# Kernel tuning notes

Measured on AMD Instinct MI355X. Metric: run time of the kernel, lower is better.

The kernel has to match this reference:

```python
import jax, jax.numpy as jnp
import numpy as np

D_MODEL = 256
N_HEADS = 8
N_LEVELS = 4
N_POINTS = 4
SHAPES = np.array([[64, 64], [32, 32], [16, 16], [8, 8]], dtype=np.int32)


def setup_inputs() -> dict:
    key = jax.random.key(0)
    ks = jax.random.split(key, 10)
    Lq = int((SHAPES[:, 0] * SHAPES[:, 1]).sum())  # 5440
    N, d = 8, D_MODEL
    noff = N_HEADS * N_LEVELS * N_POINTS * 2
    nw = N_HEADS * N_LEVELS * N_POINTS
    s = 1.0 / np.sqrt(d).astype(np.float32)
    inp = {
        'query': jax.random.normal(ks[0], (N, Lq, d), jnp.float32),
        'reference_points': jax.random.uniform(ks[1], (N, Lq, N_LEVELS, 2), jnp.float32),
        'spatial_shapes': jnp.asarray(SHAPES),
        'level_start_index': jnp.asarray(np.concatenate([[0], np.cumsum(SHAPES[:, 0] * SHAPES[:, 1])[:-1]]).astype(np.int32)),
        'W_value': jax.random.normal(ks[2], (d, d), jnp.float32) * s,
        'b_value': jnp.zeros((d,), jnp.float32),
        'W_off': jax.random.normal(ks[3], (d, noff), jnp.float32) * 0.01,
        'b_off': jax.random.uniform(ks[4], (noff,), jnp.float32, minval=-0.5, maxval=0.5),
        'W_attn': jax.random.normal(ks[5], (d, nw), jnp.float32) * s,
        'b_attn': jnp.zeros((nw,), jnp.float32),
        'W_out': jax.random.normal(ks[6], (d, d), jnp.float32) * s,
        'b_out': jnp.zeros((d,), jnp.float32),
    }
    return inp


def _bilinear_sample(val_l, loc_l, H, W):
    # val_l: [N, h, H*W, dh] flattened level feature map
    # loc_l: [N, Lq, h, P, 2] normalized (x, y) in [0, 1]
    # grid_sample semantics, align_corners=False, zero padding
    N, h, HW, dh = val_l.shape
    Lq, P = loc_l.shape[1], loc_l.shape[3]
    x = loc_l[..., 0] * W - 0.5
    y = loc_l[..., 1] * H - 0.5
    x0 = jnp.floor(x)
    y0 = jnp.floor(y)
    wx = (x - x0)[..., None]  # [N, Lq, h, P, 1]
    wy = (y - y0)[..., None]
    x0i = x0.astype(jnp.int32)
    y0i = y0.astype(jnp.int32)

    def gather(yi, xi):
        valid = (xi >= 0) & (xi < W) & (yi >= 0) & (yi < H)  # [N, Lq, h, P]
        idx = jnp.clip(yi, 0, H - 1) * W + jnp.clip(xi, 0, W - 1)
        idx = idx.transpose(0, 2, 1, 3).reshape(N, h, Lq * P)  # [N, h, Lq*P]
        g = jnp.take_along_axis(val_l, jnp.broadcast_to(idx[..., None], (N, h, Lq * P, dh)), axis=2)
        g = g.reshape(N, h, Lq, P, dh)
        mask = valid.transpose(0, 2, 1, 3)[..., None].astype(val_l.dtype)
        return g * mask

    v00 = gather(y0i, x0i)
    v01 = gather(y0i, x0i + 1)
    v10 = gather(y0i + 1, x0i)
    v11 = gather(y0i + 1, x0i + 1)
    wxt = wx.transpose(0, 2, 1, 3, 4)  # [N, h, Lq, P, 1]
    wyt = wy.transpose(0, 2, 1, 3, 4)
    return (v00 * (1 - wxt) * (1 - wyt) + v01 * wxt * (1 - wyt)
            + v10 * (1 - wxt) * wyt + v11 * wxt * wyt)  # [N, h, Lq, P, dh]


def reference(query, reference_points, spatial_shapes, level_start_index,
              W_value, b_value, W_off, b_off, W_attn, b_attn, W_out, b_out):
    shapes = np.asarray(spatial_shapes)  # static level shapes
    N, Lq, d = query.shape
    h, L, P = N_HEADS, N_LEVELS, N_POINTS
    dh = d // h

    v = query @ W_value + b_value  # value_proj (source reassigns query = value_proj(query))
    off = (v @ W_off + b_off).reshape(N, Lq, h, L, P, 2)
    aw = jax.nn.softmax((v @ W_attn + b_attn).reshape(N, Lq, h, L * P), axis=-1)
    aw = aw.reshape(N, Lq, h, L, P)

    # offset_normalizer = [W_l, H_l]
    norm = jnp.asarray(np.stack([shapes[:, 1], shapes[:, 0]], -1), dtype=v.dtype)  # [L, 2]
    loc = reference_points[:, :, None, :, None, :] + off / norm[None, None, None, :, None, :]

    val = v.reshape(N, Lq, h, dh).transpose(0, 2, 1, 3)  # [N, h, Lv, dh]
    out = jnp.zeros((N, h, Lq, dh), v.dtype)
    start = 0
    for l in range(L):
        H, W = int(shapes[l, 0]), int(shapes[l, 1])
        val_l = val[:, :, start:start + H * W]
        sampled = _bilinear_sample(val_l, loc[:, :, :, l], H, W)  # [N, h, Lq, P, dh]
        w_l = aw[:, :, :, l].transpose(0, 2, 1, 3)[..., None]  # [N, h, Lq, P, 1]
        out = out + (sampled * w_l).sum(axis=3)
        start += H * W

    out = out.transpose(0, 2, 1, 3).reshape(N, Lq, d)
    return out @ W_out + b_out
```

## Files before the change

### kernel.cpp

```cpp
#include <hip/hip_runtime.h>
#include <hip/hip_bf16.h>
#include <cstdint>
#include <cstddef>

#define NB 8
#define LQ 5440
#define MROWS (NB * LQ)

typedef __attribute__((ext_vector_type(8))) _Float16       f16x8;
typedef __attribute__((ext_vector_type(4))) float          f32x4;
typedef __attribute__((ext_vector_type(8))) unsigned short ushort8_t;

__device__ __forceinline__ unsigned short f2h(float f) {
    _Float16 h = (_Float16)f;
    unsigned short u;
    __builtin_memcpy(&u, &h, 2);
    return u;
}
__device__ __forceinline__ float h2f(unsigned short u) {
    _Float16 h;
    __builtin_memcpy(&h, &u, 2);
    return (float)h;
}

__global__ __launch_bounds__(256) void prep_weights(
    const float* __restrict__ Wv, const float* __restrict__ Woff,
    const float* __restrict__ Wat, const float* __restrict__ Wo,
    unsigned short* __restrict__ WvT, unsigned short* __restrict__ WoaT,
    unsigned short* __restrict__ WoT)
{
    const int id = blockIdx.x * 256 + threadIdx.x;
    if (id < 65536) {
        const int n = id >> 8, k = id & 255;
        WvT[id] = f2h(Wv[k * 256 + n]);
    } else if (id < 65536 + 98304) {
        const int p = id - 65536;
        const int n = p >> 8, k = p & 255;
        WoaT[p] = (n < 256) ? f2h(Woff[k * 256 + n])
                            : f2h(Wat[k * 128 + (n - 256)]);
    } else {
        const int p = id - (65536 + 98304);
        const int n = p >> 8, k = p & 255;
        WoT[p] = f2h(Wo[k * 256 + n]);
    }
}

#define LDT 40

template<bool A_FP32, bool F16_OUT>
__global__ __launch_bounds__(256) void gemm_mfma(
    const void* __restrict__ Ap, const unsigned short* __restrict__ Bt,
    const float* __restrict__ bias0, const float* __restrict__ bias1,
    void* __restrict__ C0, void* __restrict__ C1,
    int cs0, int cs1, int split)
{
    __shared__ unsigned short As[128 * LDT];
    __shared__ unsigned short Bs[128 * LDT];

    const int bm = blockIdx.y * 128;
    const int bn = blockIdx.x * 128;
    const int t    = threadIdx.x;
    const int lane = t & 63;
    const int wid  = t >> 6;
    const int wm   = (wid >> 1) * 64;
    const int wn   = (wid & 1) * 64;
    const int c    = lane & 15;
    const int qq   = lane >> 4;

    const int tr = t >> 1;
    const int kh = (t & 1) * 16;

    f32x4 acc[4][4];
#pragma unroll
    for (int i = 0; i < 4; ++i)
#pragma unroll
        for (int j = 0; j < 4; ++j)
            acc[i][j] = (f32x4){0.f, 0.f, 0.f, 0.f};

    for (int k0 = 0; k0 < 256; k0 += 32) {
        if (A_FP32) {
            const float4* Af = reinterpret_cast<const float4*>(
                (const float*)Ap + (size_t)(bm + tr) * 256 + k0 + kh);
            const float4 a0 = Af[0], a1 = Af[1], a2 = Af[2], a3 = Af[3];
            ushort8_t u0, u1;
            u0[0]=f2h(a0.x); u0[1]=f2h(a0.y); u0[2]=f2h(a0.z); u0[3]=f2h(a0.w);
            u0[4]=f2h(a1.x); u0[5]=f2h(a1.y); u0[6]=f2h(a1.z); u0[7]=f2h(a1.w);
            u1[0]=f2h(a2.x); u1[1]=f2h(a2.y); u1[2]=f2h(a2.z); u1[3]=f2h(a2.w);
            u1[4]=f2h(a3.x); u1[5]=f2h(a3.y); u1[6]=f2h(a3.z); u1[7]=f2h(a3.w);
            *reinterpret_cast<ushort8_t*>(&As[tr * LDT + kh])     = u0;
            *reinterpret_cast<ushort8_t*>(&As[tr * LDT + kh + 8]) = u1;
        } else {
            const ushort8_t* Ab = reinterpret_cast<const ushort8_t*>(
                (const unsigned short*)Ap + (size_t)(bm + tr) * 256 + k0 + kh);
            *reinterpret_cast<ushort8_t*>(&As[tr * LDT + kh])     = Ab[0];
            *reinterpret_cast<ushort8_t*>(&As[tr * LDT + kh + 8]) = Ab[1];
        }
        {
            const ushort8_t* Bb = reinterpret_cast<const ushort8_t*>(
                Bt + (size_t)(bn + tr) * 256 + k0 + kh);
            *reinterpret_cast<ushort8_t*>(&Bs[tr * LDT + kh])     = Bb[0];
            *reinterpret_cast<ushort8_t*>(&Bs[tr * LDT + kh + 8]) = Bb[1];
        }
        __syncthreads();

        f16x8 af[4], bfr[4];
#pragma unroll
        for (int i = 0; i < 4; ++i)
            af[i] = *reinterpret_cast<const f16x8*>(
                &As[(wm + i * 16 + c) * LDT + qq * 8]);
#pragma unroll
        for (int j = 0; j < 4; ++j)
            bfr[j] = *reinterpret_cast<const f16x8*>(
                &Bs[(wn + j * 16 + c) * LDT + qq * 8]);
#pragma unroll
        for (int i = 0; i < 4; ++i)
#pragma unroll
            for (int j = 0; j < 4; ++j)
                acc[i][j] = __builtin_amdgcn_mfma_f32_16x16x32_f16(
                    af[i], bfr[j], acc[i][j], 0, 0, 0);
        __syncthreads();
    }

#pragma unroll
    for (int j = 0; j < 4; ++j) {
        const int col    = bn + wn + j * 16 + c;
        const bool second = col >= split;
        const int ccol   = second ? col - split : col;
        const float bv   = second ? bias1[ccol] : bias0[ccol];
#pragma unroll
        for (int i = 0; i < 4; ++i) {
#pragma unroll
            for (int r = 0; r < 4; ++r) {
                const int row = bm + wm + i * 16 + qq * 4 + r;
                const float v0 = acc[i][j][r] + bv;
                if (F16_OUT) {
                    const float v1 = __shfl_xor(v0, 1);
                    if ((lane & 1) == 0) {
                        const unsigned int packed =
                            (unsigned int)f2h(v0) | ((unsigned int)f2h(v1) << 16);
                        unsigned short* Cb = (unsigned short*)(second ? C1 : C0);
                        const int cs = second ? cs1 : cs0;
                        *reinterpret_cast<unsigned int*>(
                            Cb + (size_t)row * cs + ccol) = packed;
                    }
                } else {
                    float* Cf = (float*)C0;
                    Cf[(size_t)row * cs0 + col] = v0;
                }
            }
        }
    }
}

__global__ __launch_bounds__(256) void sample_kernel(
    const unsigned short* __restrict__ v16,
    const unsigned short* __restrict__ off16,
    const unsigned short* __restrict__ attn16,
    const float* __restrict__ refpts,
    unsigned short* __restrict__ pre16)
{
    const int lane = threadIdx.x & 63;
    const int wv   = threadIdx.x >> 6;
    const int row  = blockIdx.x * 4 + wv;
    const int n    = row / LQ;

    __shared__ float4 sW[4][136];
    __shared__ int4   sI[4][136];

    const ushort4 o4 = reinterpret_cast<const ushort4*>(off16)[(size_t)row * 64 + lane];
    const unsigned int lg = reinterpret_cast<const unsigned int*>(attn16)[(size_t)row * 64 + lane];
    const float l0 = h2f((unsigned short)(lg & 0xffff));
    const float l1 = h2f((unsigned short)(lg >> 16));

    const int h   = lane >> 3;
    const int k   = lane & 7;
    const int j0  = 2 * k;
    const int lev = j0 >> 2;
    const float rx = refpts[(size_t)row * 8 + lev * 2 + 0];
    const float ry = refpts[(size_t)row * 8 + lev * 2 + 1];

    float m = fmaxf(l0, l1);
    m = fmaxf(m, __shfl_xor(m, 1));
    m = fmaxf(m, __shfl_xor(m, 2));
    m = fmaxf(m, __shfl_xor(m, 4));
    const float e0 = __expf(l0 - m);
    const float e1 = __expf(l1 - m);
    float s = e0 + e1;
    s += __shfl_xor(s, 1);
    s += __shfl_xor(s, 2);
    s += __shfl_xor(s, 4);
    const float inv = 1.f / s;

    const int  W     = 64 >> lev;
    const int  start = (lev == 0) ? 0 : (lev == 1) ? 4096 : (lev == 2) ? 5120 : 5376;
    const float rs   = 0.015625f * (float)(1 << lev);

#pragma unroll
    for (int pp = 0; pp < 2; ++pp) {
        const float lx = rx + h2f(pp ? o4.z : o4.x) * rs;
        const float ly = ry + h2f(pp ? o4.w : o4.y) * rs;
        const float wgt = (pp ? e1 : e0) * inv;

        const float x = lx * (float)W - 0.5f;
        const float y = ly * (float)W - 0.5f;
        const float fx = floorf(x), fy = floorf(y);
        const int xi = (int)fx, yi = (int)fy;
        const float wx = x - fx, wy = y - fy;

        const int x0 = min(max(xi, 0), W - 1);
        const int x1 = min(max(xi + 1, 0), W - 1);
        const int y0 = min(max(yi, 0), W - 1);
        const int y1 = min(max(yi + 1, 0), W - 1);
        const float vx0 = (xi >= 0 && xi < W)         ? (1.f - wx) : 0.f;
        const float vx1 = (xi + 1 >= 0 && xi + 1 < W) ? wx         : 0.f;
        const float vy0 = (yi >= 0 && yi < W)         ? (1.f - wy) : 0.f;
        const float vy1 = (yi + 1 >= 0 && yi + 1 < W) ? wy         : 0.f;

        const int hb  = h * 64;
        const int b00 = (start + y0 * W + x0) * 512 + hb;
        const int b01 = (start + y0 * W + x1) * 512 + hb;
        const int b10 = (start + y1 * W + x0) * 512 + hb;
        const int b11 = (start + y1 * W + x1) * 512 + hb;

        sW[wv][h * 17 + j0 + pp] = make_float4(wgt * vy0 * vx0, wgt * vy0 * vx1,
                                               wgt * vy1 * vx0, wgt * vy1 * vx1);
        sI[wv][h * 17 + j0 + pp] = make_int4(b00, b01, b10, b11);
    }
    __syncthreads();

    const int nu = __builtin_amdgcn_readfirstlane(n);
    const char* vn = reinterpret_cast<const char*>(v16) + (size_t)nu * (LQ * 512);
    const int koff = k * 8;
    float4 acc = make_float4(0.f, 0.f, 0.f, 0.f);

#pragma unroll
    for (int j = 0; j < 16; ++j) {
        const float4 w = sW[wv][h * 17 + j];
        const int4   I = sI[wv][h * 17 + j];
        const ushort4 p00 = *reinterpret_cast<const ushort4*>(vn + (I.x + koff));
        const ushort4 p01 = *reinterpret_cast<const ushort4*>(vn + (I.y + koff));
        const ushort4 p10 = *reinterpret_cast<const ushort4*>(vn + (I.z + koff));
        const ushort4 p11 = *reinterpret_cast<const ushort4*>(vn + (I.w + koff));
        acc.x = fmaf(h2f(p00.x), w.x, acc.x);
        acc.x = fmaf(h2f(p01.x), w.y, acc.x);
        acc.x = fmaf(h2f(p10.x), w.z, acc.x);
        acc.x = fmaf(h2f(p11.x), w.w, acc.x);
        acc.y = fmaf(h2f(p00.y), w.x, acc.y);
        acc.y = fmaf(h2f(p01.y), w.y, acc.y);
        acc.y = fmaf(h2f(p10.y), w.z, acc.y);
        acc.y = fmaf(h2f(p11.y), w.w, acc.y);
        acc.z = fmaf(h2f(p00.z), w.x, acc.z);
        acc.z = fmaf(h2f(p01.z), w.y, acc.z);
        acc.z = fmaf(h2f(p10.z), w.z, acc.z);
        acc.z = fmaf(h2f(p11.z), w.w, acc.z);
        acc.w = fmaf(h2f(p00.w), w.x, acc.w);
        acc.w = fmaf(h2f(p01.w), w.y, acc.w);
        acc.w = fmaf(h2f(p10.w), w.z, acc.w);
        acc.w = fmaf(h2f(p11.w), w.w, acc.w);
    }

    ushort4 st;
    st.x = f2h(acc.x); st.y = f2h(acc.y); st.z = f2h(acc.z); st.w = f2h(acc.w);
    reinterpret_cast<ushort4*>(pre16)[(size_t)row * 64 + lane] = st;
}

extern "C" void kernel_launch(void* const* d_in, const int* in_sizes, int n_in,
                              void* d_out, int out_size, void* d_ws, size_t ws_size,
                              hipStream_t stream)
{
    const float* query   = (const float*)d_in[0];
    const float* refpts  = (const float*)d_in[1];
    const float* W_value = (const float*)d_in[4];
    const float* b_value = (const float*)d_in[5];
    const float* W_off   = (const float*)d_in[6];
    const float* b_off   = (const float*)d_in[7];
    const float* W_attn  = (const float*)d_in[8];
    const float* b_attn  = (const float*)d_in[9];
    const float* W_out   = (const float*)d_in[10];
    const float* b_out   = (const float*)d_in[11];
    float* out = (float*)d_out;

    unsigned short* ws_v16   = (unsigned short*)d_ws;
    unsigned short* ws_off16 = ws_v16   + (size_t)MROWS * 256;
    unsigned short* ws_at16  = ws_off16 + (size_t)MROWS * 256;
    unsigned short* ws_pre16 = ws_at16  + (size_t)MROWS * 128;
    unsigned short* ws_wvT   = ws_pre16 + (size_t)MROWS * 256;
    unsigned short* ws_woaT  = ws_wvT   + 65536;
    unsigned short* ws_woT   = ws_woaT  + 98304;

    prep_weights<<<dim3(896), 256, 0, stream>>>(
        W_value, W_off, W_attn, W_out, ws_wvT, ws_woaT, ws_woT);

    gemm_mfma<true, true><<<dim3(2, 340), 256, 0, stream>>>(
        query, ws_wvT, b_value, b_value, ws_v16, ws_v16, 256, 256, 1 << 30);

    gemm_mfma<false, true><<<dim3(3, 340), 256, 0, stream>>>(
        ws_v16, ws_woaT, b_off, b_attn, ws_off16, ws_at16, 256, 128, 256);

    sample_kernel<<<dim3(MROWS / 4), 256, 0, stream>>>(
        ws_v16, ws_off16, ws_at16, refpts, ws_pre16);

    gemm_mfma<false, false><<<dim3(2, 340), 256, 0, stream>>>(
        ws_pre16, ws_woT, b_out, b_out, out, out, 256, 256, 1 << 30);
}
```

Baseline: 163.9 us.

## Widen gather loads, split bilinear corners across lanes, and prefetch sample data

Reassigns lanes in the sampling kernel so each lane loads 16-byte vectors covering 8 channels for one corner row (two corners), instead of 8-byte loads covering 4 channels for all four corners. The corner-row partial sums are then combined with a cross-lane shuffle. Weights and byte offsets are packed into one shared-memory uint4 per corner pair, and the next point's loads are issued one iteration ahead. The goal is fewer, wider gather instructions and more latency hiding, at the cost of extra registers, a shuffle reduction, and only half the lanes doing the final store.

```diff
diff --git a/kernel.cpp b/kernel.cpp
--- a/kernel.cpp
+++ b/kernel.cpp
@@ -164,8 +164,7 @@
     const int row  = blockIdx.x * 4 + wv;
     const int n    = row / LQ;
 
-    __shared__ float4 sW[4][136];
-    __shared__ int4   sI[4][136];
+    __shared__ uint4 swi[4][264];
 
     const ushort4 o4 = reinterpret_cast<const ushort4*>(off16)[(size_t)row * 64 + lane];
     const unsigned int lg = reinterpret_cast<const unsigned int*>(attn16)[(size_t)row * 64 + lane];
@@ -175,7 +174,7 @@
     const int h   = lane >> 3;
     const int k   = lane & 7;
     const int j0  = 2 * k;
-    const int lev = j0 >> 2;
+    const int lev = k >> 1;
     const float rx = refpts[(size_t)row * 8 + lev * 2 + 0];
     const float ry = refpts[(size_t)row * 8 + lev * 2 + 1];
 
@@ -217,51 +216,74 @@
         const float vy1 = (yi + 1 >= 0 && yi + 1 < W) ? wy         : 0.f;
 
         const int hb  = h * 64;
-        const int b00 = (start + y0 * W + x0) * 512 + hb;
-        const int b01 = (start + y0 * W + x1) * 512 + hb;
-        const int b10 = (start + y1 * W + x0) * 512 + hb;
-        const int b11 = (start + y1 * W + x1) * 512 + hb;
-
-        sW[wv][h * 17 + j0 + pp] = make_float4(wgt * vy0 * vx0, wgt * vy0 * vx1,
-                                               wgt * vy1 * vx0, wgt * vy1 * vx1);
-        sI[wv][h * 17 + j0 + pp] = make_int4(b00, b01, b10, b11);
+        const unsigned int b00 = (unsigned int)((start + y0 * W + x0) * 512 + hb);
+        const unsigned int b01 = (unsigned int)((start + y0 * W + x1) * 512 + hb);
+        const unsigned int b10 = (unsigned int)((start + y1 * W + x0) * 512 + hb);
+        const unsigned int b11 = (unsigned int)((start + y1 * W + x1) * 512 + hb);
+
+        const int jj = j0 + pp;
+        uint4 c0, c1;
+        c0.x = __float_as_uint(wgt * vy0 * vx0);
+        c0.y = __float_as_uint(wgt * vy0 * vx1);
+        c0.z = b00; c0.w = b01;
+        c1.x = __float_as_uint(wgt * vy1 * vx0);
+        c1.y = __float_as_uint(wgt * vy1 * vx1);
+        c1.z = b10; c1.w = b11;
+        swi[wv][h * 33 + jj * 2 + 0] = c0;
+        swi[wv][h * 33 + jj * 2 + 1] = c1;
     }
     __syncthreads();
+
+    const int cp = (lane >> 2) & 1;
+    const int cg = lane & 3;
+    const unsigned int koff = cg * 16;
 
     const int nu = __builtin_amdgcn_readfirstlane(n);
     const char* vn = reinterpret_cast<const char*>(v16) + (size_t)nu * (LQ * 512);
-    const int koff = k * 8;
-    float4 acc = make_float4(0.f, 0.f, 0.f, 0.f);
+    const uint4* wib = &swi[wv][h * 33 + cp];
+
+    float acc[8];
+#pragma unroll
+    for (int i = 0; i < 8; ++i) acc[i] = 0.f;
+
+    uint4 wiA = wib[0];
+    uint4 wiB = wib[2];
+    ushort8_t vaA = *reinterpret_cast<const ushort8_t*>(vn + (wiA.z + koff));
+    ushort8_t vbA = *reinterpret_cast<const ushort8_t*>(vn + (wiA.w + koff));
 
 #pragma unroll
     for (int j = 0; j < 16; ++j) {
-        const float4 w = sW[wv][h * 17 + j];
-        const int4   I = sI[wv][h * 17 + j];
-        const ushort4 p00 = *reinterpret_cast<const ushort4*>(vn + (I.x + koff));
-        const ushort4 p01 = *reinterpret_cast<const ushort4*>(vn + (I.y + koff));
-        const ushort4 p10 = *reinterpret_cast<const ushort4*>(vn + (I.z + koff));
-        const ushort4 p11 = *reinterpret_cast<const ushort4*>(vn + (I.w + koff));
-        acc.x = fmaf(h2f(p00.x), w.x, acc.x);
-        acc.x = fmaf(h2f(p01.x), w.y, acc.x);
-        acc.x = fmaf(h2f(p10.x), w.z, acc.x);
-        acc.x = fmaf(h2f(p11.x), w.w, acc.x);
-        acc.y = fmaf(h2f(p00.y), w.x, acc.y);
-        acc.y = fmaf(h2f(p01.y), w.y, acc.y);
-        acc.y = fmaf(h2f(p10.y), w.z, acc.y);
-        acc.y = fmaf(h2f(p11.y), w.w, acc.y);
-        acc.z = fmaf(h2f(p00.z), w.x, acc.z);
-        acc.z = fmaf(h2f(p01.z), w.y, acc.z);
-        acc.z = fmaf(h2f(p10.z), w.z, acc.z);
-        acc.z = fmaf(h2f(p11.z), w.w, acc.z);
-        acc.w = fmaf(h2f(p00.w), w.x, acc.w);
-        acc.w = fmaf(h2f(p01.w), w.y, acc.w);
-        acc.w = fmaf(h2f(p10.w), w.z, acc.w);
-        acc.w = fmaf(h2f(p11.w), w.w, acc.w);
-    }
-
-    ushort4 st;
-    st.x = f2h(acc.x); st.y = f2h(acc.y); st.z = f2h(acc.z); st.w = f2h(acc.w);
-    reinterpret_cast<ushort4*>(pre16)[(size_t)row * 64 + lane] = st;
+        ushort8_t vaB, vbB;
+        if (j < 15) {
+            vaB = *reinterpret_cast<const ushort8_t*>(vn + (wiB.z + koff));
+            vbB = *reinterpret_cast<const ushort8_t*>(vn + (wiB.w + koff));
+        }
+        uint4 wiC;
+        if (j < 14) wiC = wib[2 * (j + 2)];
+
+        const float wa = __uint_as_float(wiA.x);
+        const float wb = __uint_as_float(wiA.y);
+#pragma unroll
+        for (int i = 0; i < 8; ++i)
+            acc[i] = fmaf(h2f(vaA[i]), wa, acc[i]);
+#pragma unroll
+        for (int i = 0; i < 8; ++i)
+            acc[i] = fmaf(h2f(vbA[i]), wb, acc[i]);
+
+        wiA = wiB; wiB = wiC; vaA = vaB; vbA = vbB;
+    }
+
+#pragma unroll
+    for (int i = 0; i < 8; ++i)
+        acc[i] += __shfl_xor(acc[i], 4);
+
+    if (cp == 0) {
+        ushort8_t st;
+#pragma unroll
+        for (int i = 0; i < 8; ++i) st[i] = f2h(acc[i]);
+        *reinterpret_cast<ushort8_t*>(
+            pre16 + (size_t)row * 256 + h * 32 + cg * 8) = st;
+    }
 }
 
 extern "C" void kernel_launch(void* const* d_in, const int* in_sizes, int n_in,
```

After: 143.7 us. -12.3%, faster.
